# Kernel optimization log

Hardware: AMD Instinct MI355X
Metric: run time of the kernel (lower is better)

## Reference

```python
import jax, jax.numpy as jnp
import numpy as np

NSAMPLE = 32
RADIUS = 5.0
EPS = 1e-5  # BatchNorm eps (torch default)


def setup_inputs() -> dict:
    key = jax.random.key(0)
    ks = jax.random.split(key, 8)
    B, N, C = 4, 4096, 64
    mlp = [64, 64, 64]
    inp = {
        "pos1": jax.random.normal(ks[0], (B, 3, N), jnp.float32),
        "pos2": jax.random.normal(ks[1], (B, 3, N), jnp.float32),
        "feature1": jax.random.normal(ks[2], (B, C, N), jnp.float32),
        "feature2": jax.random.normal(ks[3], (B, C, N), jnp.float32),
    }
    last = 2 * C + 3  # concat corr: feat2 + feat1 + xyz-diff
    for i, oc in enumerate(mlp):
        inp[f"W{i}"] = jax.random.normal(ks[4 + i], (oc, last), jnp.float32) / np.float32(np.sqrt(last))
        inp[f"g{i}"] = jnp.ones((oc,), jnp.float32)
        inp[f"b{i}"] = jnp.zeros((oc,), jnp.float32)
        last = oc
    return inp


def _group(f, idx):
    # f: (B, C, M), idx: (B, N, S) -> (B, C, N, S)
    return jax.vmap(lambda fb, ib: fb[:, ib])(f, idx)


def _bn_relu(x, g, b):
    # training-mode BatchNorm2d over (B, N, S) per channel, then ReLU
    m = x.mean(axis=(0, 2, 3), keepdims=True)
    v = x.var(axis=(0, 2, 3), keepdims=True)
    y = g[None, :, None, None] * (x - m) * jax.lax.rsqrt(v + EPS) + b[None, :, None, None]
    return jax.nn.relu(y)


def _forward(pos1, pos2, feature1, feature2, params):
    B, _, N = pos1.shape
    p1t = pos1.transpose(0, 2, 1)  # (B, N, 3)
    p2t = pos2.transpose(0, 2, 1)  # (B, M, 3)
    # squared pairwise distances (B, N, M)
    sq = (jnp.sum(p1t * p1t, -1, keepdims=True)
          - 2.0 * jnp.einsum('bnc,bmc->bnm', p1t, p2t)
          + jnp.sum(p2t * p2t, -1)[:, None, :])
    neg, idx = jax.lax.top_k(-sq, NSAMPLE)  # ascending-distance KNN
    dist = jnp.sqrt(jnp.maximum(-neg, 0.0))
    # replace out-of-radius neighbors with the nearest neighbor index
    idx = jnp.where(dist > RADIUS, idx[:, :, :1], idx)
    pos2_g = _group(pos2, idx)                       # (B, 3, N, S)
    pos_diff = pos2_g - pos1[:, :, :, None]
    feat2_g = _group(feature2, idx)                  # (B, C, N, S)
    feat1_rep = jnp.broadcast_to(feature1[:, :, :, None],
                                 (B, feature1.shape[1], N, NSAMPLE))
    x = jnp.concatenate([pos_diff, feat2_g, feat1_rep], axis=1)  # (B, 2C+3, N, S)
    for W, g, b in params:
        x = jnp.einsum('oc,bcns->bons', W, x)  # 1x1 conv, no bias
        x = _bn_relu(x, g, b)
    return x.max(axis=-1)  # max-pool over neighbors -> (B, mlp[-1], N)


def reference(pos1, pos2, feature1, feature2, W0, g0, b0, W1, g1, b1, W2, g2, b2):
    params = [(W0, g0, b0), (W1, g1, b1), (W2, g2, b2)]
    feat1_new = _forward(pos1, pos2, feature1, feature2, params)
    return (pos1, feat1_new)
```

## Files before the change

### kernel.cpp

```cpp
#include <hip/hip_runtime.h>
#include <hip/hip_bf16.h>


#define N_ 4096
#define S_ 32
#define PTOT 524288.0f

typedef unsigned short u16;
typedef unsigned int   u32;
typedef unsigned long long u64;
typedef __attribute__((ext_vector_type(8))) short short8;
typedef __attribute__((ext_vector_type(4))) float f32x4;

__device__ __forceinline__ float b2f(u16 u){
  union { u32 i; float f; } x; x.i = ((u32)u) << 16; return x.f;
}
__device__ __forceinline__ u16 f2b(float f){
  __hip_bfloat16 h = __float2bfloat16(f);
  return *(u16*)&h;
}
__device__ __forceinline__ u32 fenc(float f){
  u32 u = __float_as_uint(f);
  return (u & 0x80000000u) ? ~u : (u | 0x80000000u);
}
__device__ __forceinline__ float fdec(u32 k){
  return __uint_as_float((k & 0x80000000u) ? (k & 0x7FFFFFFFu) : ~k);
}
__device__ __forceinline__ int TIX(int r, int c){ return (r << 6) + (c ^ ((r & 7) << 3)); }
#define MFMA16(a,b,c) __builtin_amdgcn_mfma_f32_16x16x32_bf16((a),(b),(c),0,0,0)

__global__ void k_copy(const uint4* __restrict__ s, uint4* __restrict__ d){
  int i = blockIdx.x * 256 + threadIdx.x;
  d[i] = s[i];
}

#define PLCNT(T, OUT) { int _c = 0;                                           \
  _Pragma("unroll")                                                           \
  for (int _it = 0; _it < 64; ++_it) _c += (dl[_it] < (T)) ? 1 : 0;           \
  _Pragma("unroll")                                                           \
  for (int _d = 1; _d < 64; _d <<= 1) _c += __shfl_xor(_c, _d);               \
  OUT = (u32)_c; }

__global__ __launch_bounds__(256) void k_knn(const float* __restrict__ pos1,
        const float* __restrict__ pos2, int* __restrict__ idxb){
  __shared__ u64 lkey[4][96];
  int b = blockIdx.y;
  int l = threadIdx.x & 63;
  int w = threadIdx.x >> 6;
  int n = blockIdx.x * 4 + w;
  const float* p1 = pos1 + b * 3 * N_;
  const float* p2 = pos2 + b * 3 * N_;
  float qx = p1[n], qy = p1[N_ + n], qz = p1[2 * N_ + n];
  float dl[64];
  float minv = 3.4e38f;
  #pragma unroll
  for (int it = 0; it < 16; ++it){
    int j0 = it * 256 + l * 4;
    float4 xv = *(const float4*)(p2 + j0);
    float4 yv = *(const float4*)(p2 + N_ + j0);
    float4 zv = *(const float4*)(p2 + 2 * N_ + j0);
    float dx, dy, dz, d;
    dx=xv.x-qx; dy=yv.x-qy; dz=zv.x-qz; d=fmaf(dx,dx,fmaf(dy,dy,dz*dz)); dl[it*4+0]=d; minv=fminf(minv,d);
    dx=xv.y-qx; dy=yv.y-qy; dz=zv.y-qz; d=fmaf(dx,dx,fmaf(dy,dy,dz*dz)); dl[it*4+1]=d; minv=fminf(minv,d);
    dx=xv.z-qx; dy=yv.z-qy; dz=zv.z-qz; d=fmaf(dx,dx,fmaf(dy,dy,dz*dz)); dl[it*4+2]=d; minv=fminf(minv,d);
    dx=xv.w-qx; dy=yv.w-qy; dz=zv.w-qz; d=fmaf(dx,dx,fmaf(dy,dy,dz*dz)); dl[it*4+3]=d; minv=fminf(minv,d);
  }
  #pragma unroll
  for (int d2 = 1; d2 < 64; d2 <<= 1) minv = fminf(minv, __shfl_xor(minv, d2));
  u32 lo = __float_as_uint(minv);
  u32 hi = lo + (5u << 23); if (hi > 0x7F800000u) hi = 0x7F800000u;
  u32 step = 2u << 23;
  u32 K = 0;
  for (int e = 0; e < 12; ++e){
    PLCNT(__uint_as_float(hi), K)
    if (K >= 32u) break;
    lo = hi;
    hi += step; if (hi > 0x7F800000u) hi = 0x7F800000u;
    step <<= 1;
  }
  if (K < 32u){ hi = 0x7F800000u; PLCNT(__uint_as_float(hi), K) }
  for (int itr = 0; itr < 28 && K > 96u && (hi - lo) > 1u; ++itr){
    u32 mid = (lo + hi) >> 1, c;
    PLCNT(__uint_as_float(mid), c)
    if (c >= 32u){ hi = mid; K = c; } else lo = mid;
  }
  float T = __uint_as_float(hi);
  lkey[w][l] = ~0ull;
  if (l < 32) lkey[w][64 + l] = ~0ull;
  int myc = 0;
  #pragma unroll
  for (int it = 0; it < 64; ++it) myc += (dl[it] < T) ? 1 : 0;
  int pre = myc;
  #pragma unroll
  for (int d2 = 1; d2 < 64; d2 <<= 1){
    int t2 = __shfl_up(pre, d2); if (l >= d2) pre += t2;
  }
  int slot = pre - myc;
  for (int it = 0; it < 64; ++it){
    if (dl[it] < T){
      if (slot < 96)
        lkey[w][slot] = ((u64)__float_as_uint(dl[it]) << 32)
                      | (u32)((it >> 2) * 256 + l * 4 + (it & 3));
      slot++;
    }
  }
  int Kc = (int)(K > 96u ? 96u : K);
  u64 k0 = lkey[w][l];
  u64 k1 = (l < 32) ? lkey[w][64 + l] : ~0ull;
  int r0 = 0, r1 = 0;
  for (int j = 0; j < 96; j += 2){
    ulonglong2 kp = *(const ulonglong2*)&lkey[w][j];
    r0 += (kp.x < k0) + (kp.y < k0);
    r1 += (kp.x < k1) + (kp.y < k1);
  }
  unsigned long long m0 = __ballot((l < Kc) && (r0 == 0));
  u32 nearest;
  if (m0) nearest = (u32)__shfl((int)(u32)k0, __builtin_ctzll(m0));
  else {
    unsigned long long m1 = __ballot((l + 64 < Kc) && (r1 == 0));
    nearest = (u32)__shfl((int)(u32)k1, __builtin_ctzll(m1));
  }
  int* op = idxb + (b * N_ + n) * S_;
  float d0 = __uint_as_float((u32)(k0 >> 32));
  float d1 = __uint_as_float((u32)(k1 >> 32));
  if ((l < Kc) && (r0 < 32))      op[r0] = (d0 > 25.0f) ? (int)nearest : (int)(u32)k0;
  if ((l + 64 < Kc) && (r1 < 32)) op[r1] = (d1 > 25.0f) ? (int)nearest : (int)(u32)k1;
}

template<int MODE>
__global__ __launch_bounds__(256) void k_precomp(const float* __restrict__ posx,
        const float* __restrict__ featx, const float* __restrict__ W0,
        u16* __restrict__ outp){
  __shared__ float Ws[67][65];
  __shared__ float Xs[67][65];
  int b = blockIdx.y, j0 = blockIdx.x * 64, t = threadIdx.x;
  for (int e = t; e < 67 * 64; e += 256){
    int r = e >> 6, o = e & 63;
    int wc = (MODE == 0) ? r : (r < 3 ? r : r + 64);
    Ws[r][o] = W0[o * 131 + wc];
    float x;
    if (r < 3){ x = posx[(b * 3 + r) * N_ + j0 + o]; if (MODE) x = -x; }
    else        x = featx[(b * 64 + (r - 3)) * N_ + j0 + o];
    Xs[r][o] = x;
  }
  __syncthreads();
  int og = t & 15, sl = t >> 4;
  float acc[4][4] = {};
  for (int r = 0; r < 67; ++r){
    float w0v = Ws[r][og*4+0], w1v = Ws[r][og*4+1], w2v = Ws[r][og*4+2], w3v = Ws[r][og*4+3];
    #pragma unroll
    for (int c = 0; c < 4; ++c){
      float xv = Xs[r][sl*4+c];
      acc[c][0] += xv*w0v; acc[c][1] += xv*w1v; acc[c][2] += xv*w2v; acc[c][3] += xv*w3v;
    }
  }
  #pragma unroll
  for (int c = 0; c < 4; ++c){
    ushort4 val;
    val.x = f2b(acc[c][0]); val.y = f2b(acc[c][1]);
    val.z = f2b(acc[c][2]); val.w = f2b(acc[c][3]);
    *(ushort4*)&outp[(((size_t)(b * N_ + j0 + sl*4 + c)) << 6) + og*4] = val;
  }
}

__global__ void k_cvtW2(const float* __restrict__ W, u16* __restrict__ Wb){
  int t = threadIdx.x;
  for (int e = t; e < 4096; e += 256) Wb[e] = f2b(W[e]);
}

__global__ __launch_bounds__(256) void k_stats0(const int* __restrict__ idxb,
    const u16* __restrict__ A, const u16* __restrict__ Cn,
    float* __restrict__ sp1, float* __restrict__ sp2){
  int b = blockIdx.y, n0 = blockIdx.x * 32;
  int c4 = threadIdx.x & 15, sq = threadIdx.x >> 4;
  float4 a1 = {0,0,0,0}, a2 = {0,0,0,0};
  for (int q = 0; q < 32; ++q){
    int n = n0 + q;
    ushort4 cu = *(const ushort4*)&Cn[(((size_t)(b * N_ + n)) << 6) + c4 * 4];
    float cx = b2f(cu.x), cy = b2f(cu.y), cz = b2f(cu.z), cw = b2f(cu.w);
    const int* ip = idxb + (b * N_ + n) * 32;
    #pragma unroll
    for (int ss = 0; ss < 2; ++ss){
      int j = ip[sq + ss * 16];
      ushort4 au = *(const ushort4*)&A[(((size_t)(b * N_ + j)) << 6) + c4 * 4];
      float h0 = b2f(au.x) + cx, h1 = b2f(au.y) + cy;
      float h2 = b2f(au.z) + cz, h3 = b2f(au.w) + cw;
      a1.x += h0; a1.y += h1; a1.z += h2; a1.w += h3;
      a2.x += h0*h0; a2.y += h1*h1; a2.z += h2*h2; a2.w += h3*h3;
    }
  }
  __shared__ float red1[16][64];
  __shared__ float red2[16][64];
  *(float4*)&red1[sq][c4*4] = a1;
  *(float4*)&red2[sq][c4*4] = a2;
  __syncthreads();
  int t = threadIdx.x;
  int slot = (blockIdx.x + (blockIdx.y << 7)) & 63;
  if (t < 64){
    float s1 = 0.f, s2 = 0.f;
    #pragma unroll
    for (int k = 0; k < 16; ++k){ s1 += red1[k][t]; s2 += red2[k][t]; }
    atomicAdd(&sp1[slot * 64 + t], s1);
    atomicAdd(&sp2[slot * 64 + t], s2);
  }
}

__global__ __launch_bounds__(256) void k_bn0(const float* __restrict__ sp1,
    const float* __restrict__ sp2, const float* g, const float* bb, float* bnp){
  __shared__ float red1[4][64];
  __shared__ float red2[4][64];
  int t = threadIdx.x, c = t & 63, s = t >> 6;
  float s1 = 0.f, s2 = 0.f;
  for (int k = s * 16; k < s * 16 + 16; ++k){
    s1 += sp1[k * 64 + c]; s2 += sp2[k * 64 + c];
  }
  red1[s][c] = s1; red2[s][c] = s2;
  __syncthreads();
  if (t < 64){
    float a1 = red1[0][c] + red1[1][c] + red1[2][c] + red1[3][c];
    float a2 = red2[0][c] + red2[1][c] + red2[2][c] + red2[3][c];
    float m = a1 * (1.0f / PTOT);
    float v = a2 * (1.0f / PTOT) - m * m;
    v = v > 0.f ? v : 0.f;
    float sc = g[c] * rsqrtf(v + 1e-5f);
    bnp[c] = sc; bnp[64 + c] = bb[c] - m * sc;
  }
}

__global__ __launch_bounds__(256) void k_bnW(const float* __restrict__ W,
    const float* __restrict__ rp, const float* __restrict__ G, const float* g,
    const float* bb, float* bnp, u16* __restrict__ Wb){
  __shared__ float Ws[64][65];
  __shared__ float Gs[64][65];
  __shared__ float r_s[64];
  __shared__ float redA[4][64];
  __shared__ float redB[4][64];
  __shared__ float scs[64];
  int t = threadIdx.x, o = t & 63, s = t >> 6;
  for (int e = t; e < 4096; e += 256){
    Ws[e >> 6][e & 63] = W[e];
    Gs[e >> 6][e & 63] = G[e];
  }
  float rv = 0.f;
  for (int k = s * 32; k < s * 32 + 32; ++k) rv += rp[k * 64 + o];
  redA[s][o] = rv;
  __syncthreads();
  if (s == 0) r_s[o] = redA[0][o] + redA[1][o] + redA[2][o] + redA[3][o];
  __syncthreads();
  float pm = 0.f, pq = 0.f;
  for (int c = s * 16; c < s * 16 + 16; ++c){
    float t1 = 0.f;
    #pragma unroll
    for (int d = 0; d < 64; ++d) t1 = fmaf(Gs[c][d], Ws[o][d], t1);
    pm = fmaf(Ws[o][c], r_s[c], pm);
    pq = fmaf(Ws[o][c], t1, pq);
  }
  __syncthreads();
  redA[s][o] = pm; redB[s][o] = pq;
  __syncthreads();
  if (t < 64){
    float mean = redA[0][o] + redA[1][o] + redA[2][o] + redA[3][o];
    float qq   = redB[0][o] + redB[1][o] + redB[2][o] + redB[3][o];
    float m = mean * (1.0f / PTOT);
    float v = qq * (1.0f / PTOT) - m * m;
    v = v > 0.f ? v : 0.f;
    float sc = g[o] * rsqrtf(v + 1e-5f);
    bnp[o] = sc; bnp[64 + o] = bb[o] - m * sc;
    scs[o] = sc;
  }
  __syncthreads();
  for (int e = t; e < 4096; e += 256){
    int oo = e >> 6, cc = e & 63;
    Wb[e] = f2b(scs[oo] * Ws[oo][cc]);
  }
}

__global__ void k_reduceG(float* __restrict__ Gp, float* __restrict__ Gout){
  int e = blockIdx.x * 256 + threadIdx.x;
  float v = 0.f;
  for (int s = 0; s < 128; ++s) v += Gp[s * 4096 + e];
  Gout[e] = v;
  for (int s = 0; s < 128; ++s) Gp[s * 4096 + e] = 0.f;
}

#define GATHER_Y0(YARR)                                                       \
  int nq = n0 + ch * 2 + (l >> 5);                                            \
  int jj = idxb[((b << 12) + nq) * 32 + (l & 31)];                            \
  const u16* ap = A + (((size_t)((b << 12) + jj)) << 6) + (w << 4);           \
  const u16* cp = Cn + (((size_t)((b << 12) + nq)) << 6) + (w << 4);          \
  short8 ga0 = *(const short8*)(ap);                                          \
  short8 ga1 = *(const short8*)(ap + 8);                                      \
  short8 gc0 = *(const short8*)(cp);                                          \
  short8 gc1 = *(const short8*)(cp + 8);                                      \
  float YARR[16];                                                             \
  _Pragma("unroll")                                                           \
  for (int kk = 0; kk < 16; ++kk){                                            \
    u16 ae = (kk < 8) ? (u16)ga0[kk] : (u16)ga1[kk - 8];                      \
    u16 ce = (kk < 8) ? (u16)gc0[kk] : (u16)gc1[kk - 8];                      \
    float hv = b2f(ae) + b2f(ce);                                             \
    float sc = ((const float*)scv)[kk], sh = ((const float*)shv)[kk];         \
    YARR[kk] = fmaxf(fmaf(sc, hv, sh), 0.f);                                  \
  }

#define LOAD_BN0                                                              \
  float4 scv[4], shv[4];                                                      \
  _Pragma("unroll")                                                           \
  for (int k = 0; k < 4; ++k){                                                \
    scv[k] = *((const float4*)bnp0 + (w << 2) + k);                           \
    shv[k] = *((const float4*)bnp0 + 16 + (w << 2) + k);                      \
  }

#define LOAD_Y0IMG(CH)                                                        \
  {                                                                           \
    int rr = t >> 2, c0i = (t & 3) << 4;                                      \
    size_t gb = ((((size_t)(((blockIdx.y << 7) | blockIdx.x) << 4) + (CH)) << 12) \
                 + (rr << 6) + c0i);                                          \
    short8 e0 = *(const short8*)&y0img[gb];                                   \
    short8 e1 = *(const short8*)&y0img[gb + 8];                               \
    *(short8*)&yp[TIX(rr, c0i)] = e0;                                         \
    *(short8*)&yp[TIX(rr, c0i + 8)] = e1;                                     \
  }

template<int FAT>
__global__ __launch_bounds__(256) void k_gram0(const int* __restrict__ idxb,
    const u16* __restrict__ A, const u16* __restrict__ Cn,
    const float* __restrict__ bnp0, float* __restrict__ Gp, float* __restrict__ rp0,
    u16* __restrict__ y0img){
  __shared__ u16 yc[4096];
  __shared__ u16 yp[FAT ? 4096 : 64];
  int b = blockIdx.y, n0 = blockIdx.x * 32, t = threadIdx.x;
  int l = t & 63, w = t >> 6;
  LOAD_BN0
  f32x4 acc[4] = {};
  float rsum[16] = {};
  for (int ch = 0; ch < 16; ++ch){
    GATHER_Y0(yv)
    #pragma unroll
    for (int k = 0; k < 16; ++k){
      rsum[k] += yv[k];
      yc[TIX((w << 4) + k, l)] = f2b(yv[k]);
    }
    if (FAT){
      short8 s0v, s1v;
      #pragma unroll
      for (int i = 0; i < 8; ++i){ s0v[i] = (short)f2b(yv[i]); s1v[i] = (short)f2b(yv[8+i]); }
      *(short8*)&yp[TIX(l, (w<<4))] = s0v;
      *(short8*)&yp[TIX(l, (w<<4) + 8)] = s1v;
    }
    __syncthreads();
    #pragma unroll
    for (int ks = 0; ks < 2; ++ks){
      short8 bf = *(const short8*)&yc[TIX((w << 4) + (l & 15), ks * 32 + ((l >> 4) << 3))];
      #pragma unroll
      for (int ta = 0; ta < 4; ++ta){
        short8 af = *(const short8*)&yc[TIX(ta * 16 + (l & 15), ks * 32 + ((l >> 4) << 3))];
        acc[ta] = MFMA16(af, bf, acc[ta]);
      }
    }
    if (FAT){
      int rr = t >> 2, c0i = (t & 3) << 4;
      short8 e0 = *(const short8*)&yp[TIX(rr, c0i)];
      short8 e1 = *(const short8*)&yp[TIX(rr, c0i + 8)];
      size_t gb = ((((size_t)(((blockIdx.y << 7) | blockIdx.x) << 4) + ch) << 12)
                   + (rr << 6) + c0i);
      *(short8*)&y0img[gb] = e0;
      *(short8*)&y0img[gb + 8] = e1;
    }
    __syncthreads();
  }
  int slot = ((blockIdx.x << 2) + blockIdx.y) & 127;
  float* gp = Gp + slot * 4096;
  #pragma unroll
  for (int ta = 0; ta < 4; ++ta)
    #pragma unroll
    for (int r = 0; r < 4; ++r)
      atomicAdd(&gp[(ta*16 + ((l>>4)<<2) + r) * 64 + (w<<4) + (l & 15)], acc[ta][r]);
  #pragma unroll
  for (int i = 0; i < 16; ++i){
    float v = rsum[i];
    #pragma unroll
    for (int s = 32; s >= 1; s >>= 1) v += __shfl_xor(v, s);
    if (l == 0) atomicAdd(&rp0[slot * 64 + (w<<4) + i], v);
  }
}

template<int FAT>
__global__ __launch_bounds__(256) void k_gram1(const int* __restrict__ idxb,
    const u16* __restrict__ A, const u16* __restrict__ Cn,
    const float* __restrict__ bnp0, const u16* __restrict__ W1b,
    const u16* __restrict__ W2r, const float* __restrict__ bnp1,
    float* __restrict__ Gp, float* __restrict__ rp1,
    const u16* __restrict__ y0img, float* __restrict__ mraw){
  __shared__ u16 yp[4096];
  __shared__ u16 y1c[4096];
  __shared__ u16 y1p[4096];
  __shared__ u32 omax[2048];
  __shared__ float sh1[64];
  __shared__ float rsh[64];
  int b = blockIdx.y, n0 = blockIdx.x * 32, t = threadIdx.x;
  int l = t & 63, w = t >> 6;
  LOAD_BN0
  if (t < 64){ sh1[t] = bnp1[64 + t]; rsh[t] = 0.f; }
  for (int e = t; e < 2048; e += 256) omax[e] = 0u;
  short8 wf[4][2], wf2[4][2];
  #pragma unroll
  for (int to = 0; to < 4; ++to)
    #pragma unroll
    for (int ks = 0; ks < 2; ++ks){
      wf[to][ks]  = *(const short8*)&W1b[(to*16 + (l & 15)) * 64 + ks*32 + ((l>>4)<<3)];
      wf2[to][ks] = *(const short8*)&W2r[(to*16 + (l & 15)) * 64 + ks*32 + ((l>>4)<<3)];
    }
  __syncthreads();
  float sh1v[4][4];
  #pragma unroll
  for (int to = 0; to < 4; ++to)
    #pragma unroll
    for (int r = 0; r < 4; ++r)
      sh1v[to][r] = sh1[to*16 + ((l>>4)<<2) + r];
  f32x4 gacc[4] = {};
  float rs[4][4] = {};
  for (int ch = 0; ch < 16; ++ch){
    if (FAT){
      LOAD_Y0IMG(ch)
    } else {
      GATHER_Y0(yv)
      short8 s0, s1;
      #pragma unroll
      for (int i = 0; i < 8; ++i){ s0[i] = (short)f2b(yv[i]); s1[i] = (short)f2b(yv[8+i]); }
      *(short8*)&yp[TIX(l, (w<<4))] = s0;
      *(short8*)&yp[TIX(l, (w<<4) + 8)] = s1;
    }
    __syncthreads();
    short8 bf0 = *(const short8*)&yp[TIX((w<<4) + (l & 15), ((l>>4)<<3))];
    short8 bf1 = *(const short8*)&yp[TIX((w<<4) + (l & 15), 32 + ((l>>4)<<3))];
    f32x4 h[4] = {};
    #pragma unroll
    for (int to = 0; to < 4; ++to){
      h[to] = MFMA16(wf[to][0], bf0, h[to]);
      h[to] = MFMA16(wf[to][1], bf1, h[to]);
    }
    int pcol = (w<<4) + (l & 15);
    #pragma unroll
    for (int to = 0; to < 4; ++to){
      ushort4 sv;
      #pragma unroll
      for (int r = 0; r < 4; ++r){
        int o = to*16 + ((l>>4)<<2) + r;
        float y = h[to][r] + sh1v[to][r];
        y = y > 0.f ? y : 0.f;
        rs[to][r] += y;
        u16 yb = f2b(y);
        y1c[TIX(o, pcol)] = yb;
        ((u16*)&sv)[r] = yb;
      }
      *(ushort4*)&y1p[TIX(pcol, to*16 + ((l>>4)<<2))] = sv;
    }
    __syncthreads();
    #pragma unroll
    for (int ks = 0; ks < 2; ++ks){
      short8 bf = *(const short8*)&y1c[TIX((w<<4) + (l & 15), ks*32 + ((l>>4)<<3))];
      #pragma unroll
      for (int ta = 0; ta < 4; ++ta){
        short8 af = *(const short8*)&y1c[TIX(ta*16 + (l & 15), ks*32 + ((l>>4)<<3))];
        gacc[ta] = MFMA16(af, bf, gacc[ta]);
      }
    }
    short8 c0 = *(const short8*)&y1p[TIX(pcol, ((l>>4)<<3))];
    short8 c1 = *(const short8*)&y1p[TIX(pcol, 32 + ((l>>4)<<3))];
    f32x4 h2[4] = {};
    #pragma unroll
    for (int to = 0; to < 4; ++to){
      h2[to] = MFMA16(wf2[to][0], c0, h2[to]);
      h2[to] = MFMA16(wf2[to][1], c1, h2[to]);
    }
    int qloc = ch * 2 + (w >> 1);
    #pragma unroll
    for (int to = 0; to < 4; ++to)
      #pragma unroll
      for (int r = 0; r < 4; ++r){
        float m = h2[to][r];
        #pragma unroll
        for (int s = 1; s <= 8; s <<= 1) m = fmaxf(m, __shfl_xor(m, s));
        if ((l & 15) == 0)
          atomicMax(&omax[qloc*64 + to*16 + ((l>>4)<<2) + r], fenc(m));
      }
    __syncthreads();
  }
  int slot = ((blockIdx.x << 2) + blockIdx.y) & 127;
  float* gp = Gp + slot * 4096;
  #pragma unroll
  for (int ta = 0; ta < 4; ++ta)
    #pragma unroll
    for (int r = 0; r < 4; ++r)
      atomicAdd(&gp[(ta*16 + ((l>>4)<<2) + r) * 64 + (w<<4) + (l & 15)], gacc[ta][r]);
  #pragma unroll
  for (int to = 0; to < 4; ++to)
    #pragma unroll
    for (int r = 0; r < 4; ++r){
      float v = rs[to][r];
      #pragma unroll
      for (int s = 1; s <= 8; s <<= 1) v += __shfl_xor(v, s);
      if ((l & 15) == 0) atomicAdd(&rsh[to*16 + ((l>>4)<<2) + r], v);
    }
  __syncthreads();
  if (t < 64) atomicAdd(&rp1[slot * 64 + t], rsh[t]);
  for (int e = t; e < 2048; e += 256){
    int q = e >> 6, o = e & 63;
    mraw[(((size_t)((b << 12) + n0 + q)) << 6) + o] = fdec(omax[e]);
  }
}

__global__ __launch_bounds__(256) void k_epi(const float* __restrict__ mraw,
    const float* __restrict__ bnp2, float* __restrict__ outp){
  __shared__ float tile[64][65];
  int b = blockIdx.y, n0 = blockIdx.x * 64, t = threadIdx.x;
  int o = t & 63, w = t >> 6;
  float sc = bnp2[o], sh = bnp2[64 + o];
  #pragma unroll
  for (int i = 0; i < 16; ++i){
    int n = i * 4 + w;
    float m = mraw[(((size_t)((b << 12) + n0 + n)) << 6) + o];
    float y = fmaf(sc, m, sh);
    tile[n][o] = y > 0.f ? y : 0.f;
  }
  __syncthreads();
  #pragma unroll
  for (int i = 0; i < 16; ++i){
    int oo = i * 4 + w;
    outp[49152 + ((size_t)((b << 6) + oo)) * N_ + n0 + o] = tile[o][oo];
  }
}

extern "C" void kernel_launch(void* const* d_in, const int* in_sizes, int n_in,
                              void* d_out, int out_size, void* d_ws, size_t ws_size,
                              hipStream_t stream){
  (void)in_sizes; (void)n_in; (void)out_size;
  const float* pos1 = (const float*)d_in[0];
  const float* pos2 = (const float*)d_in[1];
  const float* f1   = (const float*)d_in[2];
  const float* f2   = (const float*)d_in[3];
  const float* W0   = (const float*)d_in[4];
  const float* g0   = (const float*)d_in[5];
  const float* b0   = (const float*)d_in[6];
  const float* W1   = (const float*)d_in[7];
  const float* g1   = (const float*)d_in[8];
  const float* b1   = (const float*)d_in[9];
  const float* W2   = (const float*)d_in[10];
  const float* g2   = (const float*)d_in[11];
  const float* b2   = (const float*)d_in[12];

  char* ws = (char*)d_ws;
  int*   idxb = (int*)ws;
  u16*   A    = (u16*)(ws + (2u << 20));
  u16*   Cn   = (u16*)(ws + (4u << 20));
  float* Gp   = (float*)(ws + (6u << 20));
  float* st2  = (float*)(ws + (8u << 20));
  float* rp0  = st2;
  float* rp1  = st2 + 8192;
  float* sp1  = st2 + 16384;
  float* sp2  = st2 + 20480;
  float* G0   = st2 + 24576;
  float* G1   = st2 + 28672;
  float* bnp0 = st2 + 32768;
  float* bnp1 = bnp0 + 128;
  float* bnp2 = bnp1 + 128;
  u16*   W1b  = (u16*)(st2 + 33152);
  u16*   W2b  = (u16*)(st2 + 35200);
  u16*   W2r  = (u16*)(st2 + 37248);
  float* mraw = (float*)(ws + (9u << 20));
  u16*   y0img = (u16*)(ws + (16u << 20));
  bool fat = ws_size >= ((size_t)96 << 20);

  hipMemsetAsync(Gp, 0, (2u << 20) + 98304u, stream);

  k_copy<<<dim3(48), 256, 0, stream>>>((const uint4*)pos1, (uint4*)d_out);
  k_knn<<<dim3(1024, 4), 256, 0, stream>>>(pos1, pos2, idxb);
  k_precomp<0><<<dim3(64, 4), 256, 0, stream>>>(pos2, f2, W0, A);
  k_precomp<1><<<dim3(64, 4), 256, 0, stream>>>(pos1, f1, W0, Cn);
  k_cvtW2<<<dim3(1), 256, 0, stream>>>(W2, W2r);
  k_stats0<<<dim3(128, 4), 256, 0, stream>>>(idxb, A, Cn, sp1, sp2);
  k_bn0<<<dim3(1), 256, 0, stream>>>(sp1, sp2, g0, b0, bnp0);
  if (fat){
    k_gram0<1><<<dim3(128, 4), 256, 0, stream>>>(idxb, A, Cn, bnp0, Gp, rp0, y0img);
    k_reduceG<<<dim3(16), 256, 0, stream>>>(Gp, G0);
    k_bnW<<<dim3(1), 256, 0, stream>>>(W1, rp0, G0, g1, b1, bnp1, W1b);
    k_gram1<1><<<dim3(128, 4), 256, 0, stream>>>(idxb, A, Cn, bnp0, W1b, W2r, bnp1,
                                                 Gp, rp1, y0img, mraw);
    k_reduceG<<<dim3(16), 256, 0, stream>>>(Gp, G1);
    k_bnW<<<dim3(1), 256, 0, stream>>>(W2, rp1, G1, g2, b2, bnp2, W2b);
  } else {
    k_gram0<0><<<dim3(128, 4), 256, 0, stream>>>(idxb, A, Cn, bnp0, Gp, rp0, y0img);
    k_reduceG<<<dim3(16), 256, 0, stream>>>(Gp, G0);
    k_bnW<<<dim3(1), 256, 0, stream>>>(W1, rp0, G0, g1, b1, bnp1, W1b);
    k_gram1<0><<<dim3(128, 4), 256, 0, stream>>>(idxb, A, Cn, bnp0, W1b, W2r, bnp1,
                                                 Gp, rp1, y0img, mraw);
    k_reduceG<<<dim3(16), 256, 0, stream>>>(Gp, G1);
    k_bnW<<<dim3(1), 256, 0, stream>>>(W2, rp1, G1, g2, b2, bnp2, W2b);
  }
  k_epi<<<dim3(64, 4), 256, 0, stream>>>(mraw, bnp2, (float*)d_out);
}
```

Baseline: 273.4 us.

## Double block size in stats and gram kernels, splitting chunks across two warp groups

k_stats0, k_gram0 and k_gram1 now launch 512 threads per block. The two 256-thread groups work on alternating neighbor chunks, each with its own shared-memory buffers. Their partial Gram accumulators are combined in shared memory before a single set of global atomics. The aim is more in-flight work per block to hide gather latency and fewer global atomics per block. In exchange, shared memory per block doubles, which may limit occupancy, and a reduction sync is added.

```diff
diff --git a/kernel.cpp b/kernel.cpp
--- a/kernel.cpp
+++ b/kernel.cpp
@@ -168,13 +168,14 @@
   for (int e = t; e < 4096; e += 256) Wb[e] = f2b(W[e]);
 }
 
-__global__ __launch_bounds__(256) void k_stats0(const int* __restrict__ idxb,
+__global__ __launch_bounds__(512, 4) void k_stats0(const int* __restrict__ idxb,
     const u16* __restrict__ A, const u16* __restrict__ Cn,
     float* __restrict__ sp1, float* __restrict__ sp2){
   int b = blockIdx.y, n0 = blockIdx.x * 32;
-  int c4 = threadIdx.x & 15, sq = threadIdx.x >> 4;
+  int t = threadIdx.x;
+  int c4 = t & 15, sq = (t >> 4) & 15, g = t >> 8;
   float4 a1 = {0,0,0,0}, a2 = {0,0,0,0};
-  for (int q = 0; q < 32; ++q){
+  for (int q = g * 16; q < g * 16 + 16; ++q){
     int n = n0 + q;
     ushort4 cu = *(const ushort4*)&Cn[(((size_t)(b * N_ + n)) << 6) + c4 * 4];
     float cx = b2f(cu.x), cy = b2f(cu.y), cz = b2f(cu.z), cw = b2f(cu.w);
@@ -189,17 +190,16 @@
       a2.x += h0*h0; a2.y += h1*h1; a2.z += h2*h2; a2.w += h3*h3;
     }
   }
-  __shared__ float red1[16][64];
-  __shared__ float red2[16][64];
-  *(float4*)&red1[sq][c4*4] = a1;
-  *(float4*)&red2[sq][c4*4] = a2;
-  __syncthreads();
-  int t = threadIdx.x;
+  __shared__ float red1[32][64];
+  __shared__ float red2[32][64];
+  *(float4*)&red1[g*16 + sq][c4*4] = a1;
+  *(float4*)&red2[g*16 + sq][c4*4] = a2;
+  __syncthreads();
   int slot = (blockIdx.x + (blockIdx.y << 7)) & 63;
   if (t < 64){
     float s1 = 0.f, s2 = 0.f;
     #pragma unroll
-    for (int k = 0; k < 16; ++k){ s1 += red1[k][t]; s2 += red2[k][t]; }
+    for (int k = 0; k < 32; ++k){ s1 += red1[k][t]; s2 += red2[k][t]; }
     atomicAdd(&sp1[slot * 64 + t], s1);
     atomicAdd(&sp2[slot * 64 + t], s2);
   }
@@ -286,8 +286,8 @@
 #define GATHER_Y0(YARR)                                                       \
   int nq = n0 + ch * 2 + (l >> 5);                                            \
   int jj = idxb[((b << 12) + nq) * 32 + (l & 31)];                            \
-  const u16* ap = A + (((size_t)((b << 12) + jj)) << 6) + (w << 4);           \
-  const u16* cp = Cn + (((size_t)((b << 12) + nq)) << 6) + (w << 4);          \
+  const u16* ap = A + (((size_t)((b << 12) + jj)) << 6) + (wl << 4);          \
+  const u16* cp = Cn + (((size_t)((b << 12) + nq)) << 6) + (wl << 4);         \
   short8 ga0 = *(const short8*)(ap);                                          \
   short8 ga1 = *(const short8*)(ap + 8);                                      \
   short8 gc0 = *(const short8*)(cp);                                          \
@@ -306,61 +306,54 @@
   float4 scv[4], shv[4];                                                      \
   _Pragma("unroll")                                                           \
   for (int k = 0; k < 4; ++k){                                                \
-    scv[k] = *((const float4*)bnp0 + (w << 2) + k);                           \
-    shv[k] = *((const float4*)bnp0 + 16 + (w << 2) + k);                      \
-  }
-
-#define LOAD_Y0IMG(CH)                                                        \
-  {                                                                           \
-    int rr = t >> 2, c0i = (t & 3) << 4;                                      \
-    size_t gb = ((((size_t)(((blockIdx.y << 7) | blockIdx.x) << 4) + (CH)) << 12) \
-                 + (rr << 6) + c0i);                                          \
-    short8 e0 = *(const short8*)&y0img[gb];                                   \
-    short8 e1 = *(const short8*)&y0img[gb + 8];                               \
-    *(short8*)&yp[TIX(rr, c0i)] = e0;                                         \
-    *(short8*)&yp[TIX(rr, c0i + 8)] = e1;                                     \
+    scv[k] = *((const float4*)bnp0 + (wl << 2) + k);                          \
+    shv[k] = *((const float4*)bnp0 + 16 + (wl << 2) + k);                     \
   }
 
 template<int FAT>
-__global__ __launch_bounds__(256) void k_gram0(const int* __restrict__ idxb,
+__global__ __launch_bounds__(512, 4) void k_gram0(const int* __restrict__ idxb,
     const u16* __restrict__ A, const u16* __restrict__ Cn,
     const float* __restrict__ bnp0, float* __restrict__ Gp, float* __restrict__ rp0,
     u16* __restrict__ y0img){
-  __shared__ u16 yc[4096];
-  __shared__ u16 yp[FAT ? 4096 : 64];
+  __shared__ u16 yc[8192];
+  __shared__ u16 yp[FAT ? 8192 : 128];
   int b = blockIdx.y, n0 = blockIdx.x * 32, t = threadIdx.x;
   int l = t & 63, w = t >> 6;
+  int g = w >> 2, wl = w & 3;
+  int tg = (wl << 6) | l;
+  int go = g << 12;
   LOAD_BN0
   f32x4 acc[4] = {};
   float rsum[16] = {};
-  for (int ch = 0; ch < 16; ++ch){
+  for (int chb = 0; chb < 16; chb += 2){
+    int ch = chb + g;
     GATHER_Y0(yv)
     #pragma unroll
     for (int k = 0; k < 16; ++k){
       rsum[k] += yv[k];
-      yc[TIX((w << 4) + k, l)] = f2b(yv[k]);
+      yc[go + TIX((wl << 4) + k, l)] = f2b(yv[k]);
     }
     if (FAT){
       short8 s0v, s1v;
       #pragma unroll
       for (int i = 0; i < 8; ++i){ s0v[i] = (short)f2b(yv[i]); s1v[i] = (short)f2b(yv[8+i]); }
-      *(short8*)&yp[TIX(l, (w<<4))] = s0v;
-      *(short8*)&yp[TIX(l, (w<<4) + 8)] = s1v;
+      *(short8*)&yp[go + TIX(l, (wl<<4))] = s0v;
+      *(short8*)&yp[go + TIX(l, (wl<<4) + 8)] = s1v;
     }
     __syncthreads();
     #pragma unroll
     for (int ks = 0; ks < 2; ++ks){
-      short8 bf = *(const short8*)&yc[TIX((w << 4) + (l & 15), ks * 32 + ((l >> 4) << 3))];
+      short8 bf = *(const short8*)&yc[go + TIX((wl << 4) + (l & 15), ks * 32 + ((l >> 4) << 3))];
       #pragma unroll
       for (int ta = 0; ta < 4; ++ta){
-        short8 af = *(const short8*)&yc[TIX(ta * 16 + (l & 15), ks * 32 + ((l >> 4) << 3))];
+        short8 af = *(const short8*)&yc[go + TIX(ta * 16 + (l & 15), ks * 32 + ((l >> 4) << 3))];
         acc[ta] = MFMA16(af, bf, acc[ta]);
       }
     }
     if (FAT){
-      int rr = t >> 2, c0i = (t & 3) << 4;
-      short8 e0 = *(const short8*)&yp[TIX(rr, c0i)];
-      short8 e1 = *(const short8*)&yp[TIX(rr, c0i + 8)];
+      int rr = tg >> 2, c0i = (tg & 3) << 4;
+      short8 e0 = *(const short8*)&yp[go + TIX(rr, c0i)];
+      short8 e1 = *(const short8*)&yp[go + TIX(rr, c0i + 8)];
       size_t gb = ((((size_t)(((blockIdx.y << 7) | blockIdx.x) << 4) + ch) << 12)
                    + (rr << 6) + c0i);
       *(short8*)&y0img[gb] = e0;
@@ -371,37 +364,53 @@
   int slot = ((blockIdx.x << 2) + blockIdx.y) & 127;
   float* gp = Gp + slot * 4096;
   #pragma unroll
-  for (int ta = 0; ta < 4; ++ta)
-    #pragma unroll
-    for (int r = 0; r < 4; ++r)
-      atomicAdd(&gp[(ta*16 + ((l>>4)<<2) + r) * 64 + (w<<4) + (l & 15)], acc[ta][r]);
-  #pragma unroll
   for (int i = 0; i < 16; ++i){
     float v = rsum[i];
     #pragma unroll
     for (int s = 32; s >= 1; s >>= 1) v += __shfl_xor(v, s);
-    if (l == 0) atomicAdd(&rp0[slot * 64 + (w<<4) + i], v);
+    if (l == 0) atomicAdd(&rp0[slot * 64 + (wl<<4) + i], v);
+  }
+  float* redG = (float*)yc;
+  if (g == 1){
+    #pragma unroll
+    for (int ta = 0; ta < 4; ++ta)
+      #pragma unroll
+      for (int r = 0; r < 4; ++r)
+        redG[(ta*16 + ((l>>4)<<2) + r) * 64 + (wl<<4) + (l & 15)] = acc[ta][r];
+  }
+  __syncthreads();
+  if (g == 0){
+    #pragma unroll
+    for (int ta = 0; ta < 4; ++ta)
+      #pragma unroll
+      for (int r = 0; r < 4; ++r){
+        int ix = (ta*16 + ((l>>4)<<2) + r) * 64 + (wl<<4) + (l & 15);
+        atomicAdd(&gp[ix], acc[ta][r] + redG[ix]);
+      }
   }
 }
 
 template<int FAT>
-__global__ __launch_bounds__(256) void k_gram1(const int* __restrict__ idxb,
+__global__ __launch_bounds__(512, 4) void k_gram1(const int* __restrict__ idxb,
     const u16* __restrict__ A, const u16* __restrict__ Cn,
     const float* __restrict__ bnp0, const u16* __restrict__ W1b,
     const u16* __restrict__ W2r, const float* __restrict__ bnp1,
     float* __restrict__ Gp, float* __restrict__ rp1,
     const u16* __restrict__ y0img, float* __restrict__ mraw){
-  __shared__ u16 yp[4096];
-  __shared__ u16 y1c[4096];
-  __shared__ u16 y1p[4096];
+  __shared__ u16 yp[8192];
+  __shared__ u16 y1c[8192];
+  __shared__ u16 y1p[8192];
   __shared__ u32 omax[2048];
   __shared__ float sh1[64];
   __shared__ float rsh[64];
   int b = blockIdx.y, n0 = blockIdx.x * 32, t = threadIdx.x;
   int l = t & 63, w = t >> 6;
+  int g = w >> 2, wl = w & 3;
+  int tg = (wl << 6) | l;
+  int go = g << 12;
   LOAD_BN0
   if (t < 64){ sh1[t] = bnp1[64 + t]; rsh[t] = 0.f; }
-  for (int e = t; e < 2048; e += 256) omax[e] = 0u;
+  for (int e = t; e < 2048; e += 512) omax[e] = 0u;
   short8 wf[4][2], wf2[4][2];
   #pragma unroll
   for (int to = 0; to < 4; ++to)
@@ -419,27 +428,34 @@
       sh1v[to][r] = sh1[to*16 + ((l>>4)<<2) + r];
   f32x4 gacc[4] = {};
   float rs[4][4] = {};
-  for (int ch = 0; ch < 16; ++ch){
+  for (int chb = 0; chb < 16; chb += 2){
+    int ch = chb + g;
     if (FAT){
-      LOAD_Y0IMG(ch)
+      int rr = tg >> 2, c0i = (tg & 3) << 4;
+      size_t gb = ((((size_t)(((blockIdx.y << 7) | blockIdx.x) << 4) + ch) << 12)
+                   + (rr << 6) + c0i);
+      short8 e0 = *(const short8*)&y0img[gb];
+      short8 e1 = *(const short8*)&y0img[gb + 8];
+      *(short8*)&yp[go + TIX(rr, c0i)] = e0;
+      *(short8*)&yp[go + TIX(rr, c0i + 8)] = e1;
     } else {
       GATHER_Y0(yv)
       short8 s0, s1;
       #pragma unroll
       for (int i = 0; i < 8; ++i){ s0[i] = (short)f2b(yv[i]); s1[i] = (short)f2b(yv[8+i]); }
-      *(short8*)&yp[TIX(l, (w<<4))] = s0;
-      *(short8*)&yp[TIX(l, (w<<4) + 8)] = s1;
+      *(short8*)&yp[go + TIX(l, (wl<<4))] = s0;
+      *(short8*)&yp[go + TIX(l, (wl<<4) + 8)] = s1;
     }
     __syncthreads();
-    short8 bf0 = *(const short8*)&yp[TIX((w<<4) + (l & 15), ((l>>4)<<3))];
-    short8 bf1 = *(const short8*)&yp[TIX((w<<4) + (l & 15), 32 + ((l>>4)<<3))];
+    short8 bf0 = *(const short8*)&yp[go + TIX((wl<<4) + (l & 15), ((l>>4)<<3))];
+    short8 bf1 = *(const short8*)&yp[go + TIX((wl<<4) + (l & 15), 32 + ((l>>4)<<3))];
     f32x4 h[4] = {};
     #pragma unroll
     for (int to = 0; to < 4; ++to){
       h[to] = MFMA16(wf[to][0], bf0, h[to]);
       h[to] = MFMA16(wf[to][1], bf1, h[to]);
     }
-    int pcol = (w<<4) + (l & 15);
+    int pcol = (wl<<4) + (l & 15);
     #pragma unroll
     for (int to = 0; to < 4; ++to){
       ushort4 sv;
@@ -450,30 +466,30 @@
         y = y > 0.f ? y : 0.f;
         rs[to][r] += y;
         u16 yb = f2b(y);
-        y1c[TIX(o, pcol)] = yb;
+        y1c[go + TIX(o, pcol)] = yb;
         ((u16*)&sv)[r] = yb;
       }
-      *(ushort4*)&y1p[TIX(pcol, to*16 + ((l>>4)<<2))] = sv;
+      *(ushort4*)&y1p[go + TIX(pcol, to*16 + ((l>>4)<<2))] = sv;
     }
     __syncthreads();
     #pragma unroll
     for (int ks = 0; ks < 2; ++ks){
-      short8 bf = *(const short8*)&y1c[TIX((w<<4) + (l & 15), ks*32 + ((l>>4)<<3))];
+      short8 bf = *(const short8*)&y1c[go + TIX((wl<<4) + (l & 15), ks*32 + ((l>>4)<<3))];
       #pragma unroll
       for (int ta = 0; ta < 4; ++ta){
-        short8 af = *(const short8*)&y1c[TIX(ta*16 + (l & 15), ks*32 + ((l>>4)<<3))];
+        short8 af = *(const short8*)&y1c[go + TIX(ta*16 + (l & 15), ks*32 + ((l>>4)<<3))];
         gacc[ta] = MFMA16(af, bf, gacc[ta]);
       }
     }
-    short8 c0 = *(const short8*)&y1p[TIX(pcol, ((l>>4)<<3))];
-    short8 c1 = *(const short8*)&y1p[TIX(pcol, 32 + ((l>>4)<<3))];
+    short8 c0 = *(const short8*)&y1p[go + TIX(pcol, ((l>>4)<<3))];
+    short8 c1 = *(const short8*)&y1p[go + TIX(pcol, 32 + ((l>>4)<<3))];
     f32x4 h2[4] = {};
     #pragma unroll
     for (int to = 0; to < 4; ++to){
       h2[to] = MFMA16(wf2[to][0], c0, h2[to]);
       h2[to] = MFMA16(wf2[to][1], c1, h2[to]);
     }
-    int qloc = ch * 2 + (w >> 1);
+    int qloc = ch * 2 + (wl >> 1);
     #pragma unroll
     for (int to = 0; to < 4; ++to)
       #pragma unroll
@@ -489,11 +505,6 @@
   int slot = ((blockIdx.x << 2) + blockIdx.y) & 127;
   float* gp = Gp + slot * 4096;
   #pragma unroll
-  for (int ta = 0; ta < 4; ++ta)
-    #pragma unroll
-    for (int r = 0; r < 4; ++r)
-      atomicAdd(&gp[(ta*16 + ((l>>4)<<2) + r) * 64 + (w<<4) + (l & 15)], gacc[ta][r]);
-  #pragma unroll
   for (int to = 0; to < 4; ++to)
     #pragma unroll
     for (int r = 0; r < 4; ++r){
@@ -502,9 +513,26 @@
       for (int s = 1; s <= 8; s <<= 1) v += __shfl_xor(v, s);
       if ((l & 15) == 0) atomicAdd(&rsh[to*16 + ((l>>4)<<2) + r], v);
     }
-  __syncthreads();
+  float* redG = (float*)yp;
+  if (g == 1){
+    #pragma unroll
+    for (int ta = 0; ta < 4; ++ta)
+      #pragma unroll
+      for (int r = 0; r < 4; ++r)
+        redG[(ta*16 + ((l>>4)<<2) + r) * 64 + (wl<<4) + (l & 15)] = gacc[ta][r];
+  }
+  __syncthreads();
+  if (g == 0){
+    #pragma unroll
+    for (int ta = 0; ta < 4; ++ta)
+      #pragma unroll
+      for (int r = 0; r < 4; ++r){
+        int ix = (ta*16 + ((l>>4)<<2) + r) * 64 + (wl<<4) + (l & 15);
+        atomicAdd(&gp[ix], gacc[ta][r] + redG[ix]);
+      }
+  }
   if (t < 64) atomicAdd(&rp1[slot * 64 + t], rsh[t]);
-  for (int e = t; e < 2048; e += 256){
+  for (int e = t; e < 2048; e += 512){
     int q = e >> 6, o = e & 63;
     mraw[(((size_t)((b << 12) + n0 + q)) << 6) + o] = fdec(omax[e]);
   }
@@ -578,21 +606,21 @@
   k_precomp<0><<<dim3(64, 4), 256, 0, stream>>>(pos2, f2, W0, A);
   k_precomp<1><<<dim3(64, 4), 256, 0, stream>>>(pos1, f1, W0, Cn);
   k_cvtW2<<<dim3(1), 256, 0, stream>>>(W2, W2r);
-  k_stats0<<<dim3(128, 4), 256, 0, stream>>>(idxb, A, Cn, sp1, sp2);
+  k_stats0<<<dim3(128, 4), 512, 0, stream>>>(idxb, A, Cn, sp1, sp2);
   k_bn0<<<dim3(1), 256, 0, stream>>>(sp1, sp2, g0, b0, bnp0);
   if (fat){
-    k_gram0<1><<<dim3(128, 4), 256, 0, stream>>>(idxb, A, Cn, bnp0, Gp, rp0, y0img);
+    k_gram0<1><<<dim3(128, 4), 512, 0, stream>>>(idxb, A, Cn, bnp0, Gp, rp0, y0img);
     k_reduceG<<<dim3(16), 256, 0, stream>>>(Gp, G0);
     k_bnW<<<dim3(1), 256, 0, stream>>>(W1, rp0, G0, g1, b1, bnp1, W1b);
-    k_gram1<1><<<dim3(128, 4), 256, 0, stream>>>(idxb, A, Cn, bnp0, W1b, W2r, bnp1,
+    k_gram1<1><<<dim3(128, 4), 512, 0, stream>>>(idxb, A, Cn, bnp0, W1b, W2r, bnp1,
                                                  Gp, rp1, y0img, mraw);
     k_reduceG<<<dim3(16), 256, 0, stream>>>(Gp, G1);
     k_bnW<<<dim3(1), 256, 0, stream>>>(W2, rp1, G1, g2, b2, bnp2, W2b);
   } else {
-    k_gram0<0><<<dim3(128, 4), 256, 0, stream>>>(idxb, A, Cn, bnp0, Gp, rp0, y0img);
+    k_gram0<0><<<dim3(128, 4), 512, 0, stream>>>(idxb, A, Cn, bnp0, Gp, rp0, y0img);
     k_reduceG<<<dim3(16), 256, 0, stream>>>(Gp, G0);
     k_bnW<<<dim3(1), 256, 0, stream>>>(W1, rp0, G0, g1, b1, bnp1, W1b);
-    k_gram1<0><<<dim3(128, 4), 256, 0, stream>>>(idxb, A, Cn, bnp0, W1b, W2r, bnp1,
+    k_gram1<0><<<dim3(128, 4), 512, 0, stream>>>(idxb, A, Cn, bnp0, W1b, W2r, bnp1,
                                                  Gp, rp1, y0img, mraw);
     k_reduceG<<<dim3(16), 256, 0, stream>>>(Gp, G1);
     k_bnW<<<dim3(1), 256, 0, stream>>>(W2, rp1, G1, g2, b2, bnp2, W2b);
```

Result: slower. 315.5 us (+15.4%).
